# Kernel optimization log

Measured on AMD Instinct MI355X. Metric: run time of the kernel, lower is better.

The kernel has to match this reference:

```python
import jax, jax.numpy as jnp
import numpy as np

BAND_WIDTH = 0.5
EPS = 1e-5


def setup_inputs() -> dict:
    key = jax.random.key(0)
    k1, k2 = jax.random.split(key)
    shape = (8, 128, 16, 16, 16)  # (N, C, H, W, D)
    x = jax.random.normal(k1, shape, dtype=jnp.float32)
    y = jax.random.normal(k2, shape, dtype=jnp.float32)
    return {"x": x, "y": y}


def reference(x, y):
    N, C = x.shape[0], x.shape[1]
    L = x.shape[2] * x.shape[3] * x.shape[4]  # H*W*D
    xr = x.reshape(N, C, L)
    yr = y.reshape(N, C, L)
    # center by target mean over (batch, spatial)
    y_mu = yr.mean(axis=(0, 2), keepdims=True)  # (1, C, 1)
    xc = xr - y_mu
    yc = yr - y_mu
    # L2 normalize along channel dim (torch F.normalize: eps=1e-12 clamp on norm)
    xn = xc / jnp.maximum(jnp.linalg.norm(xc, axis=1, keepdims=True), 1e-12)
    yn = yc / jnp.maximum(jnp.linalg.norm(yc, axis=1, keepdims=True), 1e-12)
    # cosine similarity matrix (N, L, L): rows index x positions, cols y positions
    cos = jnp.einsum('ncl,ncm->nlm', xn, yn)
    dist = 1.0 - cos
    dist_min = jnp.min(dist, axis=2, keepdims=True)  # (N, L, 1)
    dist_tilde = dist / (dist_min + EPS)
    cx = jax.nn.softmax((1.0 - dist_tilde) / BAND_WIDTH, axis=2)
    cx = jnp.mean(jnp.max(cx, axis=1), axis=1)  # (N,)
    loss = jnp.mean(-jnp.log(cx + EPS))
    return loss
```

## Files before the change

kernel.cpp:

```cpp
#include <hip/hip_runtime.h>
#include <math.h>


#define NB 8
#define CC 128
#define LL 4096
#define CL (CC * LL)
#define EPSV 1e-5f
#define L2E 1.44269504f

typedef __bf16 bf16x8 __attribute__((ext_vector_type(8)));
typedef float f32x4 __attribute__((ext_vector_type(4)));

__device__ __forceinline__ unsigned short f2bf(float f) {
    unsigned u = __float_as_uint(f);
    u += 0x7FFFu + ((u >> 16) & 1u);
    return (unsigned short)(u >> 16);
}

__global__ void k_mu1(const float* __restrict__ y, float* __restrict__ muP) {
    const int b = blockIdx.x;
    const int t = threadIdx.x;
    const float* p = y + (size_t)b * LL;
    float4 v0 = *(const float4*)(p + t * 4);
    float4 v1 = *(const float4*)(p + 1024 + t * 4);
    float4 v2 = *(const float4*)(p + 2048 + t * 4);
    float4 v3 = *(const float4*)(p + 3072 + t * 4);
    float s = (v0.x + v0.y + v0.z + v0.w) + (v1.x + v1.y + v1.z + v1.w)
            + (v2.x + v2.y + v2.z + v2.w) + (v3.x + v3.y + v3.z + v3.w);
    for (int o = 1; o < 64; o <<= 1) s += __shfl_xor(s, o, 64);
    __shared__ float red[4];
    if ((t & 63) == 0) red[t >> 6] = s;
    __syncthreads();
    if (t == 0) muP[b] = (red[0] + red[1]) + (red[2] + red[3]);
}

__global__ void k_mu2(const float* __restrict__ muP, float* __restrict__ mu, float* __restrict__ out) {
    const int c = threadIdx.x;
    float s = 0.f;
#pragma unroll
    for (int n = 0; n < NB; ++n) s += muP[n * CC + c];
    mu[c] = s * (1.0f / (float)(NB * LL));
    if (c == 0) out[0] = 0.f;
}

__global__ __launch_bounds__(256, 2) void k_prep(const float* __restrict__ x, const float* __restrict__ y,
                                                 const float* __restrict__ mu,
                                                 unsigned short* __restrict__ xt, unsigned short* __restrict__ yt) {
    __shared__ float tf[CC][132];
    __shared__ float ssq[2][CC];
    __shared__ float invn[CC];
    const int b = blockIdx.x;
    const float* src = (b & 256) ? y : x;
    unsigned short* dst = (b & 256) ? yt : xt;
    const int sub = b & 255;
    const int n = sub >> 5, l0 = (sub & 31) << 7;
    const int t = threadIdx.x;
    const float* g = src + (size_t)n * CL + l0;
#pragma unroll
    for (int it = 0; it < 16; ++it) {
        int id = (it << 8) + t;
        int c = id >> 5, l4 = (id & 31) << 2;
        *(float4*)&tf[c][l4] = *(const float4*)(g + (size_t)c * LL + l4);
    }
    __syncthreads();
    {
        const int l = t & 127, half = t >> 7;
        float ss = 0.f;
#pragma unroll
        for (int cc = 0; cc < 64; ++cc) {
            int c = (half << 6) + cc;
            float v = tf[c][l] - mu[c];
            tf[c][l] = v;
            ss += v * v;
        }
        ssq[half][l] = ss;
    }
    __syncthreads();
    if (t < CC) invn[t] = 1.0f / fmaxf(sqrtf(ssq[0][t] + ssq[1][t]), 1e-12f);
    __syncthreads();
    unsigned short* o = dst + ((size_t)n * LL + l0) * CC;
#pragma unroll
    for (int it = 0; it < 8; ++it) {
        int id = (it << 8) + t;
        int lr = id >> 4, c8 = (id & 15) << 3;
        float w = invn[lr];
        unsigned short h[8] __attribute__((aligned(16)));
#pragma unroll
        for (int j = 0; j < 8; ++j) h[j] = f2bf(tf[c8 + j][lr] * w);
        *(uint4*)&o[(size_t)lr * CC + c8] = *(uint4*)h;
    }
}

__device__ __forceinline__ void stage_dma(const unsigned short* __restrict__ g,
                                          unsigned short* lds, int t) {
    const int w = t >> 6, ln = t & 63;
#pragma unroll
    for (int c = 0; c < 8; ++c) {
        int rbase = w * 32 + c * 4;
        int row = rbase + (ln >> 4);
        int gg = (ln & 15) ^ (row & 15);
        const unsigned short* gp = g + ((size_t)row << 7) + (gg << 3);
        __builtin_amdgcn_global_load_lds(
            (const __attribute__((address_space(1))) void*)gp,
            (__attribute__((address_space(3))) void*)(lds + (rbase << 7)),
            16, 0, 0);
    }
}

__device__ __forceinline__ bf16x8 ldsfrag(const unsigned short* lds, int r, int kq) {
    return *(const bf16x8*)&lds[(r << 7) + ((kq ^ (r & 15)) << 3)];
}

__device__ __forceinline__ void gather_frags(const unsigned short* __restrict__ g,
                                             bf16x8 (&areg)[4][4], int row0, int lane) {
    const int mr = lane & 15, q = lane >> 4;
    const unsigned short* ab = g + ((size_t)(row0 + mr) << 7) + q * 8;
#pragma unroll
    for (int k0i = 0; k0i < 4; ++k0i)
#pragma unroll
        for (int i = 0; i < 4; ++i)
            areg[k0i][i] = *(const bf16x8*)(ab + ((size_t)(i * 16) << 7) + k0i * 32);
}

__device__ __forceinline__ void mfma_stream(const bf16x8 (&areg)[4][4], const unsigned short* Bs,
                                            f32x4 (&acc)[4][4], int col0, int lane) {
    const int mr = lane & 15, q = lane >> 4;
#pragma unroll
    for (int k0i = 0; k0i < 4; ++k0i) {
        bf16x8 b[4];
#pragma unroll
        for (int j = 0; j < 4; ++j)
            b[j] = ldsfrag(Bs, col0 + j * 16 + mr, 4 * k0i + q);
#pragma unroll
        for (int i = 0; i < 4; ++i)
#pragma unroll
            for (int j = 0; j < 4; ++j)
                acc[i][j] = __builtin_amdgcn_mfma_f32_16x16x32_bf16(areg[k0i][i], b[j], acc[i][j], 0, 0, 0);
    }
}


#define DECODE_B(b, n_, lt_, ms_)                          \
    const int xcd_ = (b) & 7, slot_ = (b) >> 3;            \
    const int grp_ = xcd_ * 4 + (slot_ >> 5);              \
    const int n_ = grp_ >> 2, ms_ = grp_ & 3, lt_ = slot_ & 31;

__global__ __launch_bounds__(256, 2) void k_rowmax(const unsigned short* __restrict__ xt,
                                                   const unsigned short* __restrict__ yt,
                                                   float* __restrict__ rmP) {
    __shared__ unsigned short Bs[CC * CC];
    DECODE_B(blockIdx.x, n, lt, ms)
    const int t = threadIdx.x, lane = t & 63, w = t >> 6;
    const int row0 = (w & 1) << 6, col0 = (w >> 1) << 6;
    const int q = lane >> 4;
    bf16x8 areg[4][4];
    gather_frags(xt + ((size_t)(n * LL + lt * 128) << 7), areg, row0, lane);
    float rmax[16];
#pragma unroll
    for (int v = 0; v < 16; ++v) rmax[v] = -1e30f;
    for (int mt = ms * 8; mt < ms * 8 + 8; ++mt) {
        __syncthreads();
        stage_dma(yt + ((size_t)(n * LL + mt * 128) << 7), Bs, t);
        __syncthreads();
        f32x4 acc[4][4];
#pragma unroll
        for (int i = 0; i < 4; ++i)
#pragma unroll
            for (int j = 0; j < 4; ++j) acc[i][j] = 0.f;
        mfma_stream(areg, Bs, acc, col0, lane);
#pragma unroll
        for (int i = 0; i < 4; ++i)
#pragma unroll
            for (int r = 0; r < 4; ++r) {
                float m = acc[i][0][r];
#pragma unroll
                for (int j = 1; j < 4; ++j) m = fmaxf(m, acc[i][j][r]);
                rmax[i * 4 + r] = fmaxf(rmax[i * 4 + r], m);
            }
    }
#pragma unroll
    for (int v = 0; v < 16; ++v) {
        rmax[v] = fmaxf(rmax[v], __shfl_xor(rmax[v], 1, 64));
        rmax[v] = fmaxf(rmax[v], __shfl_xor(rmax[v], 2, 64));
        rmax[v] = fmaxf(rmax[v], __shfl_xor(rmax[v], 4, 64));
        rmax[v] = fmaxf(rmax[v], __shfl_xor(rmax[v], 8, 64));
    }
    if ((lane & 15) == 0) {
        const int part = ms * 2 + (w >> 1);
#pragma unroll
        for (int v = 0; v < 16; ++v) {
            int row = lt * 128 + row0 + (v >> 2) * 16 + q * 4 + (v & 3);
            rmP[((size_t)part << 15) + n * LL + row] = rmax[v];
        }
    }
}

__global__ void k_post1(const float* __restrict__ rmP, float* __restrict__ b2A, float* __restrict__ e2A) {
    int i = blockIdx.x * 256 + threadIdx.x;
    float rm = -1e30f;
#pragma unroll
    for (int p = 0; p < 8; ++p) rm = fmaxf(rm, rmP[i + ((size_t)p << 15)]);
    float beta = 2.0f / (1.0f - rm + EPSV);
    b2A[i] = beta * L2E;
    e2A[i] = (2.0f - beta) * L2E;
}

__global__ __launch_bounds__(256, 2) void k_z(const unsigned short* __restrict__ xt,
                                              const unsigned short* __restrict__ yt,
                                              const float* __restrict__ b2A, const float* __restrict__ e2A,
                                              float* __restrict__ Zp) {
    __shared__ unsigned short Bs[CC * CC];
    DECODE_B(blockIdx.x, n, lt, ms)
    const int t = threadIdx.x, lane = t & 63, w = t >> 6;
    const int row0 = (w & 1) << 6, col0 = (w >> 1) << 6;
    const int q = lane >> 4;
    bf16x8 areg[4][4];
    gather_frags(xt + ((size_t)(n * LL + lt * 128) << 7), areg, row0, lane);
    float b2[16], e2[16], zs[16];
#pragma unroll
    for (int v = 0; v < 16; ++v) {
        int row = lt * 128 + row0 + (v >> 2) * 16 + q * 4 + (v & 3);
        b2[v] = b2A[n * LL + row];
        e2[v] = e2A[n * LL + row];
        zs[v] = 0.f;
    }
    for (int mt = ms * 8; mt < ms * 8 + 8; ++mt) {
        __syncthreads();
        stage_dma(yt + ((size_t)(n * LL + mt * 128) << 7), Bs, t);
        __syncthreads();
        f32x4 acc[4][4];
#pragma unroll
        for (int i = 0; i < 4; ++i)
#pragma unroll
            for (int j = 0; j < 4; ++j) acc[i][j] = 0.f;
        mfma_stream(areg, Bs, acc, col0, lane);
#pragma unroll
        for (int i = 0; i < 4; ++i)
#pragma unroll
            for (int r = 0; r < 4; ++r) {
                int v = i * 4 + r;
                float s = 0.f;
#pragma unroll
                for (int j = 0; j < 4; ++j)
                    s += __builtin_amdgcn_exp2f(fmaf(b2[v], acc[i][j][r], e2[v]));
                zs[v] += s;
            }
    }
#pragma unroll
    for (int v = 0; v < 16; ++v) {
        zs[v] += __shfl_xor(zs[v], 1, 64);
        zs[v] += __shfl_xor(zs[v], 2, 64);
        zs[v] += __shfl_xor(zs[v], 4, 64);
        zs[v] += __shfl_xor(zs[v], 8, 64);
    }
    if ((lane & 15) == 0) {
        const int part = ms * 2 + (w >> 1);
#pragma unroll
        for (int v = 0; v < 16; ++v) {
            int row = lt * 128 + row0 + (v >> 2) * 16 + q * 4 + (v & 3);
            Zp[((size_t)part << 15) + n * LL + row] = zs[v];
        }
    }
}

__global__ void k_post2(const float* __restrict__ Zp, const float* __restrict__ e2A,
                        float* __restrict__ g2A) {
    int i = blockIdx.x * 256 + threadIdx.x;
    float Z = 0.f;
#pragma unroll
    for (int p = 0; p < 8; ++p) Z += Zp[i + ((size_t)p << 15)];
    g2A[i] = e2A[i] - __builtin_amdgcn_logf(Z);
}

__global__ __launch_bounds__(256, 2) void k_colmax(const unsigned short* __restrict__ xt,
                                                   const unsigned short* __restrict__ yt,
                                                   const float* __restrict__ b2A, const float* __restrict__ g2A,
                                                   float* __restrict__ cmP) {
    __shared__ unsigned short Bs[CC * CC];
    DECODE_B(blockIdx.x, n, ct, ls)
    const int t = threadIdx.x, lane = t & 63, w = t >> 6;
    const int row0 = (w & 1) << 6, col0 = (w >> 1) << 6;
    const int mr = lane & 15, q = lane >> 4;
    bf16x8 areg[4][4];
    gather_frags(yt + ((size_t)(n * LL + ct * 128) << 7), areg, row0, lane);
    float cmax[16];
#pragma unroll
    for (int v = 0; v < 16; ++v) cmax[v] = -1e30f;
    for (int lt = ls * 8; lt < ls * 8 + 8; ++lt) {
        __syncthreads();
        stage_dma(xt + ((size_t)(n * LL + lt * 128) << 7), Bs, t);
        __syncthreads();
        f32x4 acc[4][4];
#pragma unroll
        for (int i = 0; i < 4; ++i)
#pragma unroll
            for (int j = 0; j < 4; ++j) acc[i][j] = 0.f;
        mfma_stream(areg, Bs, acc, col0, lane);
        float b2v[4], g2v[4];
#pragma unroll
        for (int j = 0; j < 4; ++j) {
            int xr = lt * 128 + col0 + j * 16 + mr;
            b2v[j] = b2A[n * LL + xr];
            g2v[j] = g2A[n * LL + xr];
        }
#pragma unroll
        for (int i = 0; i < 4; ++i)
#pragma unroll
            for (int r = 0; r < 4; ++r) {
                int v = i * 4 + r;
                float m = cmax[v];
#pragma unroll
                for (int j = 0; j < 4; ++j)
                    m = fmaxf(m, fmaf(b2v[j], acc[i][j][r], g2v[j]));
                cmax[v] = m;
            }
    }
#pragma unroll
    for (int v = 0; v < 16; ++v) {
        cmax[v] = fmaxf(cmax[v], __shfl_xor(cmax[v], 1, 64));
        cmax[v] = fmaxf(cmax[v], __shfl_xor(cmax[v], 2, 64));
        cmax[v] = fmaxf(cmax[v], __shfl_xor(cmax[v], 4, 64));
        cmax[v] = fmaxf(cmax[v], __shfl_xor(cmax[v], 8, 64));
    }
    if (mr == 0) {
        const int part = ls * 2 + (w >> 1);
#pragma unroll
        for (int v = 0; v < 16; ++v) {
            int yc = ct * 128 + row0 + (v >> 2) * 16 + q * 4 + (v & 3);
            cmP[((size_t)part << 15) + n * LL + yc] = cmax[v];
        }
    }
}

__global__ void k_loss(const float* __restrict__ cmP, float* __restrict__ out) {
    __shared__ float red[256];
    const int n = blockIdx.x, t = threadIdx.x;
    float s = 0.f;
    for (int m = t; m < LL; m += 256) {
        size_t idx = (size_t)n * LL + m;
        float e = -1e30f;
#pragma unroll
        for (int p = 0; p < 8; ++p) e = fmaxf(e, cmP[idx + ((size_t)p << 15)]);
        s += __builtin_amdgcn_exp2f(e);
    }
    red[t] = s;
    __syncthreads();
    for (int o = 128; o > 0; o >>= 1) {
        if (t < o) red[t] += red[t + o];
        __syncthreads();
    }
    if (t == 0)
        atomicAdd(out, -logf(red[0] * (1.0f / (float)LL) + EPSV) * (1.0f / (float)NB));
}

extern "C" void kernel_launch(void* const* d_in, const int* in_sizes, int n_in,
                              void* d_out, int out_size, void* d_ws, size_t ws_size,
                              hipStream_t stream) {
    const float* x = (const float*)d_in[0];
    const float* y = (const float*)d_in[1];
    float* out = (float*)d_out;
    char* ws = (char*)d_ws;

    unsigned short* xt = (unsigned short*)ws;
    unsigned short* yt = (unsigned short*)(ws + 8388608);
    char* p = ws + 16777216;
    float* mu  = (float*)p;            p += 512;
    float* muP = (float*)p;            p += 4096;
    float* b2A = (float*)p;            p += 131072;
    float* e2A = (float*)p;            p += 131072;
    float* g2A = (float*)p;            p += 131072;
    float* rmP = (float*)p;            p += 8 * 131072;
    float* Zp  = (float*)p;            p += 8 * 131072;
    float* cmP = rmP;

    k_mu1<<<1024, 256, 0, stream>>>(y, muP);
    k_mu2<<<1, 128, 0, stream>>>(muP, mu, out);
    k_prep<<<512, 256, 0, stream>>>(x, y, mu, xt, yt);
    k_rowmax<<<1024, 256, 0, stream>>>(xt, yt, rmP);
    k_post1<<<128, 256, 0, stream>>>(rmP, b2A, e2A);
    k_z<<<1024, 256, 0, stream>>>(xt, yt, b2A, e2A, Zp);
    k_post2<<<128, 256, 0, stream>>>(Zp, e2A, g2A);
    k_colmax<<<1024, 256, 0, stream>>>(xt, yt, b2A, g2A, cmP);
    k_loss<<<8, 256, 0, stream>>>(cmP, out);
}
```

Baseline: 209.5 us.

## Reload A fragments per tile in halves to cut registers and raise occupancy

```diff
diff --git a/kernel.cpp b/kernel.cpp
--- a/kernel.cpp
+++ b/kernel.cpp
@@ -8,6 +8,7 @@
 #define CL (CC * LL)
 #define EPSV 1e-5f
 #define L2E 1.44269504f
+#define TWO_L2E 2.88539008f
 
 typedef __bf16 bf16x8 __attribute__((ext_vector_type(8)));
 typedef float f32x4 __attribute__((ext_vector_type(4)));
@@ -112,33 +113,36 @@
     return *(const bf16x8*)&lds[(r << 7) + ((kq ^ (r & 15)) << 3)];
 }
 
-__device__ __forceinline__ void gather_frags(const unsigned short* __restrict__ g,
-                                             bf16x8 (&areg)[4][4], int row0, int lane) {
+__device__ __forceinline__ void gather_half(const unsigned short* __restrict__ g,
+                                            bf16x8 (&ah)[2][4], int row0, int lane, int kh) {
     const int mr = lane & 15, q = lane >> 4;
-    const unsigned short* ab = g + ((size_t)(row0 + mr) << 7) + q * 8;
-#pragma unroll
-    for (int k0i = 0; k0i < 4; ++k0i)
-#pragma unroll
-        for (int i = 0; i < 4; ++i)
-            areg[k0i][i] = *(const bf16x8*)(ab + ((size_t)(i * 16) << 7) + k0i * 32);
-}
-
-__device__ __forceinline__ void mfma_stream(const bf16x8 (&areg)[4][4], const unsigned short* Bs,
-                                            f32x4 (&acc)[4][4], int col0, int lane) {
+    const unsigned short* ab = g + ((size_t)(row0 + mr) << 7) + kh * 64 + q * 8;
+#pragma unroll
+    for (int k2 = 0; k2 < 2; ++k2)
+#pragma unroll
+        for (int i = 0; i < 4; ++i)
+            ah[k2][i] = *(const bf16x8*)(ab + ((size_t)(i * 16) << 7) + k2 * 32);
+}
+
+__device__ __forceinline__ void mfma_half(const bf16x8 (&ah)[2][4], const unsigned short* Bs,
+                                          f32x4 (&acc)[4][4], int col0, int lane, int kh) {
     const int mr = lane & 15, q = lane >> 4;
 #pragma unroll
-    for (int k0i = 0; k0i < 4; ++k0i) {
+    for (int k2 = 0; k2 < 2; ++k2) {
+        const int kq = (kh * 2 + k2) * 4 + q;
         bf16x8 b[4];
 #pragma unroll
         for (int j = 0; j < 4; ++j)
-            b[j] = ldsfrag(Bs, col0 + j * 16 + mr, 4 * k0i + q);
+            b[j] = ldsfrag(Bs, col0 + j * 16 + mr, kq);
 #pragma unroll
         for (int i = 0; i < 4; ++i)
 #pragma unroll
             for (int j = 0; j < 4; ++j)
-                acc[i][j] = __builtin_amdgcn_mfma_f32_16x16x32_bf16(areg[k0i][i], b[j], acc[i][j], 0, 0, 0);
-    }
-}
+                acc[i][j] = __builtin_amdgcn_mfma_f32_16x16x32_bf16(ah[k2][i], b[j], acc[i][j], 0, 0, 0);
+    }
+}
+
+#define ASM_ZERO(z) int z; asm volatile("s_mov_b32 %0, 0" : "=s"(z))
 
 
 #define DECODE_B(b, n_, lt_, ms_)                          \
@@ -146,7 +150,7 @@
     const int grp_ = xcd_ * 4 + (slot_ >> 5);              \
     const int n_ = grp_ >> 2, ms_ = grp_ & 3, lt_ = slot_ & 31;
 
-__global__ __launch_bounds__(256, 2) void k_rowmax(const unsigned short* __restrict__ xt,
+__global__ __launch_bounds__(256, 3) void k_rowmax(const unsigned short* __restrict__ xt,
                                                    const unsigned short* __restrict__ yt,
                                                    float* __restrict__ rmP) {
     __shared__ unsigned short Bs[CC * CC];
@@ -154,21 +158,26 @@
     const int t = threadIdx.x, lane = t & 63, w = t >> 6;
     const int row0 = (w & 1) << 6, col0 = (w >> 1) << 6;
     const int q = lane >> 4;
-    bf16x8 areg[4][4];
-    gather_frags(xt + ((size_t)(n * LL + lt * 128) << 7), areg, row0, lane);
+    const unsigned short* fixb = xt + ((size_t)(n * LL + lt * 128) << 7);
     float rmax[16];
 #pragma unroll
     for (int v = 0; v < 16; ++v) rmax[v] = -1e30f;
+    bf16x8 ah[2][4];
     for (int mt = ms * 8; mt < ms * 8 + 8; ++mt) {
         __syncthreads();
         stage_dma(yt + ((size_t)(n * LL + mt * 128) << 7), Bs, t);
+        ASM_ZERO(z);
+        const unsigned short* fb = fixb + z;
+        gather_half(fb, ah, row0, lane, 0);
         __syncthreads();
         f32x4 acc[4][4];
 #pragma unroll
         for (int i = 0; i < 4; ++i)
 #pragma unroll
             for (int j = 0; j < 4; ++j) acc[i][j] = 0.f;
-        mfma_stream(areg, Bs, acc, col0, lane);
+        mfma_half(ah, Bs, acc, col0, lane, 0);
+        gather_half(fb, ah, row0, lane, 1);
+        mfma_half(ah, Bs, acc, col0, lane, 1);
 #pragma unroll
         for (int i = 0; i < 4; ++i)
 #pragma unroll
@@ -196,54 +205,58 @@
     }
 }
 
-__global__ void k_post1(const float* __restrict__ rmP, float* __restrict__ b2A, float* __restrict__ e2A) {
+__global__ void k_post1(const float* __restrict__ rmP, float* __restrict__ b2A) {
     int i = blockIdx.x * 256 + threadIdx.x;
     float rm = -1e30f;
 #pragma unroll
     for (int p = 0; p < 8; ++p) rm = fmaxf(rm, rmP[i + ((size_t)p << 15)]);
     float beta = 2.0f / (1.0f - rm + EPSV);
     b2A[i] = beta * L2E;
-    e2A[i] = (2.0f - beta) * L2E;
-}
-
-__global__ __launch_bounds__(256, 2) void k_z(const unsigned short* __restrict__ xt,
+}
+
+__global__ __launch_bounds__(256, 3) void k_z(const unsigned short* __restrict__ xt,
                                               const unsigned short* __restrict__ yt,
-                                              const float* __restrict__ b2A, const float* __restrict__ e2A,
+                                              const float* __restrict__ b2A,
                                               float* __restrict__ Zp) {
     __shared__ unsigned short Bs[CC * CC];
     DECODE_B(blockIdx.x, n, lt, ms)
     const int t = threadIdx.x, lane = t & 63, w = t >> 6;
     const int row0 = (w & 1) << 6, col0 = (w >> 1) << 6;
     const int q = lane >> 4;
-    bf16x8 areg[4][4];
-    gather_frags(xt + ((size_t)(n * LL + lt * 128) << 7), areg, row0, lane);
-    float b2[16], e2[16], zs[16];
+    const unsigned short* fixb = xt + ((size_t)(n * LL + lt * 128) << 7);
+    float b2[16], zs[16];
 #pragma unroll
     for (int v = 0; v < 16; ++v) {
         int row = lt * 128 + row0 + (v >> 2) * 16 + q * 4 + (v & 3);
         b2[v] = b2A[n * LL + row];
-        e2[v] = e2A[n * LL + row];
         zs[v] = 0.f;
     }
+    bf16x8 ah[2][4];
     for (int mt = ms * 8; mt < ms * 8 + 8; ++mt) {
         __syncthreads();
         stage_dma(yt + ((size_t)(n * LL + mt * 128) << 7), Bs, t);
+        ASM_ZERO(z);
+        const unsigned short* fb = fixb + z;
+        gather_half(fb, ah, row0, lane, 0);
         __syncthreads();
         f32x4 acc[4][4];
 #pragma unroll
         for (int i = 0; i < 4; ++i)
 #pragma unroll
             for (int j = 0; j < 4; ++j) acc[i][j] = 0.f;
-        mfma_stream(areg, Bs, acc, col0, lane);
+        mfma_half(ah, Bs, acc, col0, lane, 0);
+        gather_half(fb, ah, row0, lane, 1);
+        mfma_half(ah, Bs, acc, col0, lane, 1);
 #pragma unroll
         for (int i = 0; i < 4; ++i)
 #pragma unroll
             for (int r = 0; r < 4; ++r) {
                 int v = i * 4 + r;
+                float e2v = TWO_L2E - b2[v];
                 float s = 0.f;
 #pragma unroll
                 for (int j = 0; j < 4; ++j)
-                    s += __builtin_amdgcn_exp2f(fmaf(b2[v], acc[i][j][r], e2[v]));
+                    s += __builtin_amdgcn_exp2f(fmaf(b2[v], acc[i][j][r], e2v));
                 zs[v] += s;
             }
     }
@@ -264,16 +277,16 @@
     }
 }
 
-__global__ void k_post2(const float* __restrict__ Zp, const float* __restrict__ e2A,
+__global__ void k_post2(const float* __restrict__ Zp, const float* __restrict__ b2A,
                         float* __restrict__ g2A) {
     int i = blockIdx.x * 256 + threadIdx.x;
     float Z = 0.f;
 #pragma unroll
     for (int p = 0; p < 8; ++p) Z += Zp[i + ((size_t)p << 15)];
-    g2A[i] = e2A[i] - __builtin_amdgcn_logf(Z);
-}
-
-__global__ __launch_bounds__(256, 2) void k_colmax(const unsigned short* __restrict__ xt,
+    g2A[i] = (TWO_L2E - b2A[i]) - __builtin_amdgcn_logf(Z);
+}
+
+__global__ __launch_bounds__(256, 3) void k_colmax(const unsigned short* __restrict__ xt,
                                                    const unsigned short* __restrict__ yt,
                                                    const float* __restrict__ b2A, const float* __restrict__ g2A,
                                                    float* __restrict__ cmP) {
@@ -282,21 +295,26 @@
     const int t = threadIdx.x, lane = t & 63, w = t >> 6;
     const int row0 = (w & 1) << 6, col0 = (w >> 1) << 6;
     const int mr = lane & 15, q = lane >> 4;
-    bf16x8 areg[4][4];
-    gather_frags(yt + ((size_t)(n * LL + ct * 128) << 7), areg, row0, lane);
+    const unsigned short* fixb = yt + ((size_t)(n * LL + ct * 128) << 7);
     float cmax[16];
 #pragma unroll
     for (int v = 0; v < 16; ++v) cmax[v] = -1e30f;
+    bf16x8 ah[2][4];
     for (int lt = ls * 8; lt < ls * 8 + 8; ++lt) {
         __syncthreads();
         stage_dma(xt + ((size_t)(n * LL + lt * 128) << 7), Bs, t);
+        ASM_ZERO(z);
+        const unsigned short* fb = fixb + z;
+        gather_half(fb, ah, row0, lane, 0);
         __syncthreads();
         f32x4 acc[4][4];
 #pragma unroll
         for (int i = 0; i < 4; ++i)
 #pragma unroll
             for (int j = 0; j < 4; ++j) acc[i][j] = 0.f;
-        mfma_stream(areg, Bs, acc, col0, lane);
+        mfma_half(ah, Bs, acc, col0, lane, 0);
+        gather_half(fb, ah, row0, lane, 1);
+        mfma_half(ah, Bs, acc, col0, lane, 1);
         float b2v[4], g2v[4];
 #pragma unroll
         for (int j = 0; j < 4; ++j) {
@@ -368,7 +386,6 @@
     float* mu  = (float*)p;            p += 512;
     float* muP = (float*)p;            p += 4096;
     float* b2A = (float*)p;            p += 131072;
-    float* e2A = (float*)p;            p += 131072;
     float* g2A = (float*)p;            p += 131072;
     float* rmP = (float*)p;            p += 8 * 131072;
     float* Zp  = (float*)p;            p += 8 * 131072;
@@ -378,9 +395,9 @@
     k_mu2<<<1, 128, 0, stream>>>(muP, mu, out);
     k_prep<<<512, 256, 0, stream>>>(x, y, mu, xt, yt);
     k_rowmax<<<1024, 256, 0, stream>>>(xt, yt, rmP);
-    k_post1<<<128, 256, 0, stream>>>(rmP, b2A, e2A);
-    k_z<<<1024, 256, 0, stream>>>(xt, yt, b2A, e2A, Zp);
-    k_post2<<<128, 256, 0, stream>>>(Zp, e2A, g2A);
+    k_post1<<<128, 256, 0, stream>>>(rmP, b2A);
+    k_z<<<1024, 256, 0, stream>>>(xt, yt, b2A, Zp);
+    k_post2<<<128, 256, 0, stream>>>(Zp, b2A, g2A);
     k_colmax<<<1024, 256, 0, stream>>>(xt, yt, b2A, g2A, cmP);
     k_loss<<<8, 256, 0, stream>>>(cmP, out);
 }
```

Result: slower. 361.0 us (+72.3%).
